# Kernel tuning notes

Hardware: AMD Instinct MI355X
Metric: run time of the kernel (lower is better)

Reference implementation:

```python
import jax, jax.numpy as jnp
import numpy as np

N_NODES = 50000
N_EDGES = 800000
IN_CH = 128
HID = 32
HEADS = 4
OUT_CH = 64
N_GRAPHS = 64


def setup_inputs() -> dict:
    key = jax.random.key(0)
    ks = jax.random.split(key, 16)
    x = jax.random.normal(ks[0], (N_NODES, IN_CH), dtype=jnp.float32)
    edge_index = jax.random.randint(ks[1], (2, N_EDGES), 0, N_NODES, dtype=jnp.int64)
    edge_attr = jax.random.normal(ks[2], (N_EDGES, 8), dtype=jnp.float32)
    nodeIDs = jnp.sort(jax.random.randint(ks[3], (N_NODES,), 0, N_GRAPHS, dtype=jnp.int64))
    s = 0.1
    W1 = jax.random.normal(ks[4], (IN_CH, HEADS * HID), dtype=jnp.float32) * s
    att_src1 = jax.random.normal(ks[5], (HEADS, HID), dtype=jnp.float32) * s
    att_dst1 = jax.random.normal(ks[6], (HEADS, HID), dtype=jnp.float32) * s
    b1 = jax.random.normal(ks[7], (HEADS * HID,), dtype=jnp.float32) * s
    W2 = jax.random.normal(ks[8], (HEADS * HID, 16), dtype=jnp.float32) * s
    att_src2 = jax.random.normal(ks[9], (1, 16), dtype=jnp.float32) * s
    att_dst2 = jax.random.normal(ks[10], (1, 16), dtype=jnp.float32) * s
    b2 = jax.random.normal(ks[11], (16,), dtype=jnp.float32) * s
    Wf = jax.random.normal(ks[12], (16, OUT_CH), dtype=jnp.float32) * s
    bf = jax.random.normal(ks[13], (OUT_CH,), dtype=jnp.float32) * s
    return dict(x=x, edge_index=edge_index, edge_attr=edge_attr, nodeIDs=nodeIDs,
                W1=W1, att_src1=att_src1, att_dst1=att_dst1, b1=b1,
                W2=W2, att_src2=att_src2, att_dst2=att_dst2, b2=b2,
                Wf=Wf, bf=bf)


def gat_conv(x, src, dst, n, W, a_src, a_dst, b, heads, out_ch, concat):
    # linear transform -> [N, H, C]
    h = (x @ W).reshape(n, heads, out_ch)
    # per-node attention logits [N, H]
    asrc = jnp.sum(h * a_src, axis=-1)
    adst = jnp.sum(h * a_dst, axis=-1)
    e = jax.nn.leaky_relu(asrc[src] + adst[dst], 0.2)  # [E, H]
    # segment softmax over edges sharing the same destination node
    m = jax.ops.segment_max(e, dst, num_segments=n)
    e = jnp.exp(e - m[dst])
    s = jax.ops.segment_sum(e, dst, num_segments=n)
    alpha = e / (s[dst] + 1e-16)
    # weighted scatter-add aggregation: [N, H, C]
    out = jax.ops.segment_sum(alpha[:, :, None] * h[src], dst, num_segments=n)
    out = out.reshape(n, heads * out_ch) if concat else out.mean(axis=1)
    return out + b


def reference(x, edge_index, edge_attr, nodeIDs, W1, att_src1, att_dst1, b1,
              W2, att_src2, att_dst2, b2, Wf, bf):
    n = x.shape[0]
    # GATConv default: add self-loops
    loop = jnp.arange(n, dtype=edge_index.dtype)
    src = jnp.concatenate([edge_index[0], loop])
    dst = jnp.concatenate([edge_index[1], loop])
    # eval mode: dropout is identity. edge_attr ignored (no edge_dim in GATConv).
    h = jax.nn.relu(gat_conv(x, src, dst, n, W1, att_src1, att_dst1, b1, HEADS, HID, True))
    h = jax.nn.relu(gat_conv(h, src, dst, n, W2, att_src2, att_dst2, b2, 1, 16, False))
    # global mean pool over graphs
    sums = jax.ops.segment_sum(h, nodeIDs, num_segments=N_GRAPHS)
    cnts = jax.ops.segment_sum(jnp.ones((n,), dtype=h.dtype), nodeIDs, num_segments=N_GRAPHS)
    pooled = sums / jnp.maximum(cnts, 1.0)[:, None]  # [G, 16]
    return pooled @ Wf + bf
```

## Files before the change

kernel.cpp:

```cpp
#include <hip/hip_runtime.h>
#include <hip/hip_bf16.h>
#include <hip/hip_fp16.h>


__device__ __forceinline__ float lrelu02(float x) { return x > 0.f ? x : 0.2f * x; }

union H16 { _Float16 h; unsigned short u; };
__device__ __forceinline__ unsigned short f2h(float f) { H16 t; t.h = (_Float16)f; return t.u; }
__device__ __forceinline__ float h2f(unsigned short u) { H16 t; t.u = u; return (float)t.h; }

typedef __attribute__((ext_vector_type(8))) _Float16 half8v;
typedef __attribute__((ext_vector_type(4))) float f32x4;

#define CAP 64
#define CSTRIDE 16

__global__ __launch_bounds__(256) void k_bucket(
    const float* __restrict__ W1, const float* __restrict__ W2,
    unsigned short* __restrict__ W1th, unsigned short* __restrict__ W2th,
    const int* __restrict__ src, const int* __restrict__ dst,
    int* __restrict__ cnt, unsigned short* __restrict__ bkt, int E, int N)
{
    if ((int)blockIdx.x < 144) {
        if (threadIdx.x < 128) {
            int b = blockIdx.x, k = threadIdx.x;
            if (b < 128) W1th[b * 128 + k] = f2h(W1[k * 128 + b]);
            else { int c = b - 128; W2th[c * 128 + k] = f2h(W2[k * 16 + c]); }
        }
        return;
    }
    const int b  = blockIdx.x - 144;
    const int g  = b & 7;
    const int lo = (int)(((long long)N * g) >> 3);
    const int hi = (int)(((long long)N * (g + 1)) >> 3);
    const int nb = 2048 >> 3;
    const int bi = b >> 3;
    const int E4 = E >> 2;
    const int4* dst4 = (const int4*)dst;
    const int4* src4 = (const int4*)src;
    for (int i = bi * 256 + threadIdx.x; i < E4; i += nb * 256) {
        int4 d4 = dst4[i];
        int4 s4 = src4[i];
        if (d4.x >= lo && d4.x < hi) {
            int slot = atomicAdd(&cnt[d4.x * CSTRIDE], 1);
            if (slot < CAP) bkt[(d4.x << 6) + slot] = (unsigned short)s4.x;
        }
        if (d4.y >= lo && d4.y < hi) {
            int slot = atomicAdd(&cnt[d4.y * CSTRIDE], 1);
            if (slot < CAP) bkt[(d4.y << 6) + slot] = (unsigned short)s4.y;
        }
        if (d4.z >= lo && d4.z < hi) {
            int slot = atomicAdd(&cnt[d4.z * CSTRIDE], 1);
            if (slot < CAP) bkt[(d4.z << 6) + slot] = (unsigned short)s4.z;
        }
        if (d4.w >= lo && d4.w < hi) {
            int slot = atomicAdd(&cnt[d4.w * CSTRIDE], 1);
            if (slot < CAP) bkt[(d4.w << 6) + slot] = (unsigned short)s4.w;
        }
    }
    for (int i = E4 * 4 + bi * 256 + threadIdx.x; i < E; i += nb * 256) {
        int d = dst[i];
        if (d >= lo && d < hi) {
            int slot = atomicAdd(&cnt[d * CSTRIDE], 1);
            if (slot < CAP) bkt[(d << 6) + slot] = (unsigned short)src[i];
        }
    }
}

__global__ __launch_bounds__(256) void k_gemm1(
    const float* __restrict__ x, const unsigned short* __restrict__ W1th,
    const float* __restrict__ a_src, const float* __restrict__ a_dst,
    unsigned short* __restrict__ H1h, float* __restrict__ asrcv, float* __restrict__ adstv, int N)
{
    __shared__ unsigned short sL[4][16][136];
    const int tid = threadIdx.x;
    const int w  = tid >> 6, l = tid & 63;
    const int mr = l & 15, kg = l >> 4;
    const int m0 = w * 16;
    const int rowbase = blockIdx.x * 64;

    const int grow_a = rowbase + m0 + mr;
    const float* xr = x + (size_t)(grow_a < N ? grow_a : N - 1) * 128;

    f32x4 acc[8];
#pragma unroll
    for (int nt = 0; nt < 8; ++nt) acc[nt] = (f32x4){0.f, 0.f, 0.f, 0.f};

#pragma unroll
    for (int kk = 0; kk < 4; ++kk) {
        const int kbase = kk * 32 + kg * 8;
        float4 xa = *(const float4*)(xr + kbase);
        float4 xb = *(const float4*)(xr + kbase + 4);
        half8v a;
        a[0] = (_Float16)xa.x; a[1] = (_Float16)xa.y;
        a[2] = (_Float16)xa.z; a[3] = (_Float16)xa.w;
        a[4] = (_Float16)xb.x; a[5] = (_Float16)xb.y;
        a[6] = (_Float16)xb.z; a[7] = (_Float16)xb.w;
#pragma unroll
        for (int nt = 0; nt < 8; ++nt) {
            half8v b = *(const half8v*)&W1th[(size_t)(nt * 16 + mr) * 128 + kbase];
            acc[nt] = __builtin_amdgcn_mfma_f32_16x16x32_f16(a, b, acc[nt], 0, 0, 0);
        }
    }

    {
        float as_[8], ad_[8];
#pragma unroll
        for (int nt = 0; nt < 8; ++nt) { as_[nt] = a_src[nt * 16 + mr]; ad_[nt] = a_dst[nt * 16 + mr]; }
#pragma unroll
        for (int j = 0; j < 4; ++j) {
            float vs[4], vd[4];
#pragma unroll
            for (int h = 0; h < 4; ++h) {
                vs[h] = acc[2 * h][j] * as_[2 * h] + acc[2 * h + 1][j] * as_[2 * h + 1];
                vd[h] = acc[2 * h][j] * ad_[2 * h] + acc[2 * h + 1][j] * ad_[2 * h + 1];
#pragma unroll
                for (int xm = 1; xm <= 8; xm <<= 1) {
                    vs[h] += __shfl_xor(vs[h], xm);
                    vd[h] += __shfl_xor(vd[h], xm);
                }
            }
            int grow = rowbase + m0 + kg * 4 + j;
            if (mr == 0 && grow < N) {
                *(float4*)&asrcv[grow * 4] = make_float4(vs[0], vs[1], vs[2], vs[3]);
                *(float4*)&adstv[grow * 4] = make_float4(vd[0], vd[1], vd[2], vd[3]);
            }
        }
    }

#pragma unroll
    for (int nt = 0; nt < 8; ++nt)
#pragma unroll
        for (int j = 0; j < 4; ++j)
            sL[w][kg * 4 + j][nt * 16 + mr] = f2h(acc[nt][j]);
    {
        int r = l >> 2, k0 = (l & 3) * 32;
        int grow = rowbase + m0 + r;
        if (grow < N) {
            const uint4* sp = (const uint4*)&sL[w][r][k0];
            uint4* dp = (uint4*)&H1h[(size_t)grow * 128 + k0];
#pragma unroll
            for (int q = 0; q < 4; ++q) dp[q] = sp[q];
        }
    }
}

__global__ __launch_bounds__(256) void k_agg1(
    const unsigned short* __restrict__ H1h, const float* __restrict__ asrc, const float* __restrict__ adst,
    const int* __restrict__ cnt, const unsigned short* __restrict__ bkt,
    const float* __restrict__ b1, unsigned short* __restrict__ out1h, int N)
{
    __shared__ float sEs[4][64 * 4];
    __shared__ int   sSs[4][64];
    const int w = threadIdx.x >> 6, lane = threadIdx.x & 63;
    float* sE = sEs[w];
    int*   sS = sSs[w];
    const int n = blockIdx.x * 4 + w;
    if (n >= N) return;
    const int deg = min(cnt[n * CSTRIDE], CAP);

    const float4 ad4 = *(const float4*)&adst[n * 4];
    const float4 as4 = *(const float4*)&asrc[n * 4];
    float es0 = __expf(lrelu02(as4.x + ad4.x));
    float es1 = __expf(lrelu02(as4.y + ad4.y));
    float es2 = __expf(lrelu02(as4.z + ad4.z));
    float es3 = __expf(lrelu02(as4.w + ad4.w));
    float ssum0 = es0, ssum1 = es1, ssum2 = es2, ssum3 = es3;
    if (lane != 0) { ssum0 = 0.f; ssum1 = 0.f; ssum2 = 0.f; ssum3 = 0.f; }

    const int g = lane >> 4, q = lane & 15;
    const int c0 = q * 8, h = q >> 2;
    float acc[8] = {0.f,0.f,0.f,0.f,0.f,0.f,0.f,0.f};

    if (lane < deg) {
        int s = (int)bkt[(n << 6) + lane];
        sS[lane] = s;
        const float4 a = *(const float4*)&asrc[s * 4];
        float e0 = __expf(lrelu02(a.x + ad4.x));
        float e1 = __expf(lrelu02(a.y + ad4.y));
        float e2 = __expf(lrelu02(a.z + ad4.z));
        float e3 = __expf(lrelu02(a.w + ad4.w));
        ssum0 += e0; ssum1 += e1; ssum2 += e2; ssum3 += e3;
        sE[lane * 4 + 0] = e0; sE[lane * 4 + 1] = e1;
        sE[lane * 4 + 2] = e2; sE[lane * 4 + 3] = e3;
    }
    union U8 { uint4 u; _Float16 hh[8]; };
    for (int j = g; j < deg; j += 4) {
        int s = sS[j];
        float e = sE[j * 4 + h];
        U8 uu; uu.u = *(const uint4*)&H1h[(size_t)s * 128 + c0];
#pragma unroll
        for (int k = 0; k < 8; ++k)
            acc[k] = fmaf(e, (float)uu.hh[k], acc[k]);
    }

#pragma unroll
    for (int xm = 32; xm >= 1; xm >>= 1) {
        ssum0 += __shfl_xor(ssum0, xm);
        ssum1 += __shfl_xor(ssum1, xm);
        ssum2 += __shfl_xor(ssum2, xm);
        ssum3 += __shfl_xor(ssum3, xm);
    }
#pragma unroll
    for (int k = 0; k < 8; ++k) {
        acc[k] += __shfl_xor(acc[k], 16);
        acc[k] += __shfl_xor(acc[k], 32);
    }
    if (g == 0) {
        float ssv = (h == 0) ? ssum0 : (h == 1) ? ssum1 : (h == 2) ? ssum2 : ssum3;
        float esv = (h == 0) ? es0   : (h == 1) ? es1   : (h == 2) ? es2   : es3;
        float inv = 1.f / (ssv + 1e-16f);
        U8 uu; uu.u = *(const uint4*)&H1h[(size_t)n * 128 + c0];
        const float4 ba = *(const float4*)&b1[c0];
        const float4 bb = *(const float4*)&b1[c0 + 4];
        float o[8];
#pragma unroll
        for (int k = 0; k < 8; ++k) o[k] = (acc[k] + esv * (float)uu.hh[k]) * inv;
        o[0] = fmaxf(o[0] + ba.x, 0.f); o[1] = fmaxf(o[1] + ba.y, 0.f);
        o[2] = fmaxf(o[2] + ba.z, 0.f); o[3] = fmaxf(o[3] + ba.w, 0.f);
        o[4] = fmaxf(o[4] + bb.x, 0.f); o[5] = fmaxf(o[5] + bb.y, 0.f);
        o[6] = fmaxf(o[6] + bb.z, 0.f); o[7] = fmaxf(o[7] + bb.w, 0.f);
        uint2 pk0, pk1;
        pk0.x = (unsigned)f2h(o[0]) | ((unsigned)f2h(o[1]) << 16);
        pk0.y = (unsigned)f2h(o[2]) | ((unsigned)f2h(o[3]) << 16);
        pk1.x = (unsigned)f2h(o[4]) | ((unsigned)f2h(o[5]) << 16);
        pk1.y = (unsigned)f2h(o[6]) | ((unsigned)f2h(o[7]) << 16);
        *(uint2*)&out1h[(size_t)n * 128 + c0]     = pk0;
        *(uint2*)&out1h[(size_t)n * 128 + c0 + 4] = pk1;
    }
}

__global__ __launch_bounds__(256) void k_gemm2m(
    const unsigned short* __restrict__ X1h, const unsigned short* __restrict__ W2th,
    const float* __restrict__ a_src2, const float* __restrict__ a_dst2,
    unsigned short* __restrict__ H2h, float* __restrict__ asrcv, float* __restrict__ adstv, int N)
{
    const int tid = threadIdx.x;
    const int w = tid >> 6, l = tid & 63;
    const int mr = l & 15, kg = l >> 4;
    const int rowbase = blockIdx.x * 64 + w * 16;
    const int grow_a = rowbase + mr;
    const unsigned short* xr = X1h + (size_t)(grow_a < N ? grow_a : N - 1) * 128;

    f32x4 acc = (f32x4){0.f, 0.f, 0.f, 0.f};
#pragma unroll
    for (int kk = 0; kk < 4; ++kk) {
        const int kbase = kk * 32 + kg * 8;
        half8v a = *(const half8v*)&xr[kbase];
        half8v b = *(const half8v*)&W2th[mr * 128 + kbase];
        acc = __builtin_amdgcn_mfma_f32_16x16x32_f16(a, b, acc, 0, 0, 0);
    }
    const float as_ = a_src2[mr], ad_ = a_dst2[mr];
#pragma unroll
    for (int j = 0; j < 4; ++j) {
        float vs = acc[j] * as_;
        float vd = acc[j] * ad_;
#pragma unroll
        for (int xm = 1; xm <= 8; xm <<= 1) { vs += __shfl_xor(vs, xm); vd += __shfl_xor(vd, xm); }
        int grow = rowbase + kg * 4 + j;
        if (grow < N) {
            H2h[(size_t)grow * 16 + mr] = f2h(acc[j]);
            if (mr == 0) { asrcv[grow] = vs; adstv[grow] = vd; }
        }
    }
}

__global__ __launch_bounds__(256) void k_agg2(
    const unsigned short* __restrict__ H2h, const float* __restrict__ asrc, const float* __restrict__ adst,
    const int* __restrict__ cnt, const unsigned short* __restrict__ bkt,
    float* __restrict__ out, int N)
{
    __shared__ float sEs[4][64];
    __shared__ int   sSs[4][64];
    const int w = threadIdx.x >> 6, lane = threadIdx.x & 63;
    float* sE = sEs[w];
    int*   sS = sSs[w];
    const int n = blockIdx.x * 4 + w;
    if (n >= N) return;
    const int deg = min(cnt[n * CSTRIDE], CAP);

    const float adv = adst[n];
    float eself = __expf(lrelu02(asrc[n] + adv));
    float ssum = (lane == 0) ? eself : 0.f;

    const int g = lane >> 3, q = lane & 7;
    const int c0 = q * 2;
    float acc0 = 0.f, acc1 = 0.f;

    if (lane < deg) {
        int s = (int)bkt[(n << 6) + lane];
        sS[lane] = s;
        float e = __expf(lrelu02(asrc[s] + adv));
        ssum += e;
        sE[lane] = e;
    }
    union U2 { unsigned u; _Float16 hh[2]; };
    for (int j = g; j < deg; j += 8) {
        int s = sS[j];
        float e = sE[j];
        U2 uu; uu.u = *(const unsigned*)&H2h[(size_t)s * 16 + c0];
        acc0 = fmaf(e, (float)uu.hh[0], acc0);
        acc1 = fmaf(e, (float)uu.hh[1], acc1);
    }
#pragma unroll
    for (int xm = 32; xm >= 1; xm >>= 1) ssum += __shfl_xor(ssum, xm);
    acc0 += __shfl_xor(acc0, 8);  acc1 += __shfl_xor(acc1, 8);
    acc0 += __shfl_xor(acc0, 16); acc1 += __shfl_xor(acc1, 16);
    acc0 += __shfl_xor(acc0, 32); acc1 += __shfl_xor(acc1, 32);
    if (g == 0) {
        float inv = 1.f / (ssum + 1e-16f);
        U2 uu; uu.u = *(const unsigned*)&H2h[(size_t)n * 16 + c0];
        float2 o;
        o.x = (acc0 + eself * (float)uu.hh[0]) * inv;
        o.y = (acc1 + eself * (float)uu.hh[1]) * inv;
        *(float2*)&out[(size_t)n * 16 + c0] = o;
    }
}

__global__ __launch_bounds__(256) void k_poolfinal(
    const float* __restrict__ out2, const float* __restrict__ b2,
    const int* __restrict__ nodeIDs, const float* __restrict__ Wf,
    const float* __restrict__ bf, float* __restrict__ outp, int N)
{
    int g = blockIdx.x;
    int lo = 0, hi = N;
    while (lo < hi) { int mid = (lo + hi) >> 1; if (nodeIDs[mid] < g) lo = mid + 1; else hi = mid; }
    int start = lo;
    lo = 0; hi = N;
    while (lo < hi) { int mid = (lo + hi) >> 1; if (nodeIDs[mid] < g + 1) lo = mid + 1; else hi = mid; }
    int end = lo;

    int c = threadIdx.x & 15, grp = threadIdx.x >> 4;
    float bc = b2[c];
    float acc = 0.f;
    for (int n = start + grp; n < end; n += 16)
        acc += fmaxf(out2[(size_t)n * 16 + c] + bc, 0.f);

    __shared__ float sd[256];
    __shared__ float p16[16];
    sd[threadIdx.x] = acc;
    __syncthreads();
#pragma unroll
    for (int s = 8; s >= 1; s >>= 1) {
        if (grp < s) sd[threadIdx.x] += sd[(grp + s) * 16 + c];
        __syncthreads();
    }
    if (threadIdx.x < 16) {
        float cnt_ = (float)(end - start);
        p16[threadIdx.x] = sd[threadIdx.x] / fmaxf(cnt_, 1.f);
    }
    __syncthreads();
    if (threadIdx.x < 64) {
        int o = threadIdx.x;
        float a = bf[o];
#pragma unroll
        for (int k = 0; k < 16; ++k)
            a = fmaf(p16[k], Wf[k * 64 + o], a);
        outp[(size_t)g * 64 + o] = a;
    }
}

extern "C" void kernel_launch(void* const* d_in, const int* in_sizes, int n_in,
                              void* d_out, int out_size, void* d_ws, size_t ws_size,
                              hipStream_t stream)
{
    const float* x   = (const float*)d_in[0];
    const int*   ei  = (const int*)  d_in[1];
    const int*   nid = (const int*)  d_in[3];
    const float* W1  = (const float*)d_in[4];
    const float* as1 = (const float*)d_in[5];
    const float* ad1 = (const float*)d_in[6];
    const float* b1  = (const float*)d_in[7];
    const float* W2  = (const float*)d_in[8];
    const float* as2 = (const float*)d_in[9];
    const float* ad2 = (const float*)d_in[10];
    const float* b2  = (const float*)d_in[11];
    const float* Wf  = (const float*)d_in[12];
    const float* bf  = (const float*)d_in[13];
    float* outp = (float*)d_out;

    const int N = in_sizes[0] / 128;
    const int E = in_sizes[1] / 2;
    const int* src = ei;
    const int* dst = ei + E;

    char* ws = (char*)d_ws;
    size_t off_b = 0;
    auto alloc = [&](size_t bytes) -> char* {
        char* p = ws + off_b;
        off_b += (bytes + 255) & ~(size_t)255;
        return p;
    };

    unsigned short* H1h   = (unsigned short*)alloc((size_t)N * 128 * 2);
    unsigned short* out1h = (unsigned short*)alloc((size_t)N * 128 * 2);
    unsigned short* H2h   = (unsigned short*)alloc((size_t)N * 16 * 2);
    unsigned short* bkt   = (unsigned short*)alloc((size_t)N * CAP * 2);
    unsigned short* W1th  = (unsigned short*)alloc((size_t)128 * 128 * 2);
    unsigned short* W2th  = (unsigned short*)alloc((size_t)16 * 128 * 2);
    float* asrc1  = (float*)alloc((size_t)N * 4 * 4);
    float* adst1  = (float*)alloc((size_t)N * 4 * 4);
    float* out2   = (float*)alloc((size_t)N * 16 * 4);
    float* asrc2  = (float*)alloc((size_t)N * 4);
    float* adst2  = (float*)alloc((size_t)N * 4);
    int*   cnt    = (int*)  alloc((size_t)N * CSTRIDE * 4);

    auto cdiv = [](long long a, long long b) { return (int)((a + b - 1) / b); };

    const int GB = cdiv(N, 64);

    hipMemsetAsync(cnt, 0, (size_t)N * CSTRIDE * 4, stream);

    k_bucket<<<144 + 2048, 256, 0, stream>>>(W1, W2, W1th, W2th,
                                             src, dst, cnt, bkt, E, N);

    k_gemm1<<<GB, 256, 0, stream>>>(x, W1th, as1, ad1, H1h, asrc1, adst1, N);

    k_agg1<<<cdiv(N, 4), 256, 0, stream>>>(H1h, asrc1, adst1, cnt, bkt, b1, out1h, N);

    k_gemm2m<<<cdiv(N, 64), 256, 0, stream>>>(out1h, W2th, as2, ad2, H2h, asrc2, adst2, N);

    k_agg2<<<cdiv(N, 4), 256, 0, stream>>>(H2h, asrc2, adst2, cnt, bkt, out2, N);

    k_poolfinal<<<out_size / 64, 256, 0, stream>>>(out2, b2, nid, Wf, bf, outp, N);
}
```

Measured before the change: 155.7 us.

## Fuse mean-pool into layer-2 aggregation with atomics and use persistent grid-stride agg kernels

Layer-2 aggregation now applies bias and ReLU and atomically accumulates per-graph sums and counts, so the out2 buffer and the pool kernel's re-read go away. A small final kernel does the 16x64 projection. Both aggregation kernels become persistent grid-stride loops over 2048 blocks. They also pack the precomputed byte offset and the attention weight into one LDS uint2. The risk is heavy atomic contention on only 64 graphs times 16 channels, which also makes the float sum order nondeterministic.

Result: slower. 447.0 us (+187.1%).

```diff
diff --git a/kernel.cpp b/kernel.cpp
--- a/kernel.cpp
+++ b/kernel.cpp
@@ -7,7 +7,6 @@
 
 union H16 { _Float16 h; unsigned short u; };
 __device__ __forceinline__ unsigned short f2h(float f) { H16 t; t.h = (_Float16)f; return t.u; }
-__device__ __forceinline__ float h2f(unsigned short u) { H16 t; t.u = u; return (float)t.h; }
 
 typedef __attribute__((ext_vector_type(8))) _Float16 half8v;
 typedef __attribute__((ext_vector_type(4))) float f32x4;
@@ -150,83 +149,88 @@
     const int* __restrict__ cnt, const unsigned short* __restrict__ bkt,
     const float* __restrict__ b1, unsigned short* __restrict__ out1h, int N)
 {
-    __shared__ float sEs[4][64 * 4];
-    __shared__ int   sSs[4][64];
+    __shared__ uint2 sPs[4][64][4];
     const int w = threadIdx.x >> 6, lane = threadIdx.x & 63;
-    float* sE = sEs[w];
-    int*   sS = sSs[w];
-    const int n = blockIdx.x * 4 + w;
-    if (n >= N) return;
-    const int deg = min(cnt[n * CSTRIDE], CAP);
-
-    const float4 ad4 = *(const float4*)&adst[n * 4];
-    const float4 as4 = *(const float4*)&asrc[n * 4];
-    float es0 = __expf(lrelu02(as4.x + ad4.x));
-    float es1 = __expf(lrelu02(as4.y + ad4.y));
-    float es2 = __expf(lrelu02(as4.z + ad4.z));
-    float es3 = __expf(lrelu02(as4.w + ad4.w));
-    float ssum0 = es0, ssum1 = es1, ssum2 = es2, ssum3 = es3;
-    if (lane != 0) { ssum0 = 0.f; ssum1 = 0.f; ssum2 = 0.f; ssum3 = 0.f; }
-
+    uint2 (*sP)[4] = sPs[w];
     const int g = lane >> 4, q = lane & 15;
     const int c0 = q * 8, h = q >> 2;
-    float acc[8] = {0.f,0.f,0.f,0.f,0.f,0.f,0.f,0.f};
-
-    if (lane < deg) {
-        int s = (int)bkt[(n << 6) + lane];
-        sS[lane] = s;
-        const float4 a = *(const float4*)&asrc[s * 4];
-        float e0 = __expf(lrelu02(a.x + ad4.x));
-        float e1 = __expf(lrelu02(a.y + ad4.y));
-        float e2 = __expf(lrelu02(a.z + ad4.z));
-        float e3 = __expf(lrelu02(a.w + ad4.w));
-        ssum0 += e0; ssum1 += e1; ssum2 += e2; ssum3 += e3;
-        sE[lane * 4 + 0] = e0; sE[lane * 4 + 1] = e1;
-        sE[lane * 4 + 2] = e2; sE[lane * 4 + 3] = e3;
-    }
+    const int laneoff = c0 * 2;
+    const float4 ba = *(const float4*)&b1[c0];
+    const float4 bb = *(const float4*)&b1[c0 + 4];
+    const int wid = blockIdx.x * 4 + w;
+    const int nw  = gridDim.x * 4;
+    const char* H1c = (const char*)H1h;
+
     union U8 { uint4 u; _Float16 hh[8]; };
-    for (int j = g; j < deg; j += 4) {
-        int s = sS[j];
-        float e = sE[j * 4 + h];
-        U8 uu; uu.u = *(const uint4*)&H1h[(size_t)s * 128 + c0];
-#pragma unroll
-        for (int k = 0; k < 8; ++k)
-            acc[k] = fmaf(e, (float)uu.hh[k], acc[k]);
-    }
-
-#pragma unroll
-    for (int xm = 32; xm >= 1; xm >>= 1) {
-        ssum0 += __shfl_xor(ssum0, xm);
-        ssum1 += __shfl_xor(ssum1, xm);
-        ssum2 += __shfl_xor(ssum2, xm);
-        ssum3 += __shfl_xor(ssum3, xm);
-    }
-#pragma unroll
-    for (int k = 0; k < 8; ++k) {
-        acc[k] += __shfl_xor(acc[k], 16);
-        acc[k] += __shfl_xor(acc[k], 32);
-    }
-    if (g == 0) {
-        float ssv = (h == 0) ? ssum0 : (h == 1) ? ssum1 : (h == 2) ? ssum2 : ssum3;
-        float esv = (h == 0) ? es0   : (h == 1) ? es1   : (h == 2) ? es2   : es3;
-        float inv = 1.f / (ssv + 1e-16f);
-        U8 uu; uu.u = *(const uint4*)&H1h[(size_t)n * 128 + c0];
-        const float4 ba = *(const float4*)&b1[c0];
-        const float4 bb = *(const float4*)&b1[c0 + 4];
-        float o[8];
-#pragma unroll
-        for (int k = 0; k < 8; ++k) o[k] = (acc[k] + esv * (float)uu.hh[k]) * inv;
-        o[0] = fmaxf(o[0] + ba.x, 0.f); o[1] = fmaxf(o[1] + ba.y, 0.f);
-        o[2] = fmaxf(o[2] + ba.z, 0.f); o[3] = fmaxf(o[3] + ba.w, 0.f);
-        o[4] = fmaxf(o[4] + bb.x, 0.f); o[5] = fmaxf(o[5] + bb.y, 0.f);
-        o[6] = fmaxf(o[6] + bb.z, 0.f); o[7] = fmaxf(o[7] + bb.w, 0.f);
-        uint2 pk0, pk1;
-        pk0.x = (unsigned)f2h(o[0]) | ((unsigned)f2h(o[1]) << 16);
-        pk0.y = (unsigned)f2h(o[2]) | ((unsigned)f2h(o[3]) << 16);
-        pk1.x = (unsigned)f2h(o[4]) | ((unsigned)f2h(o[5]) << 16);
-        pk1.y = (unsigned)f2h(o[6]) | ((unsigned)f2h(o[7]) << 16);
-        *(uint2*)&out1h[(size_t)n * 128 + c0]     = pk0;
-        *(uint2*)&out1h[(size_t)n * 128 + c0 + 4] = pk1;
+
+    for (int n = wid; n < N; n += nw) {
+        const int deg = min(cnt[n * CSTRIDE], CAP);
+        const float4 ad4 = *(const float4*)&adst[n * 4];
+        const float4 as4 = *(const float4*)&asrc[n * 4];
+        float es0 = __expf(lrelu02(as4.x + ad4.x));
+        float es1 = __expf(lrelu02(as4.y + ad4.y));
+        float es2 = __expf(lrelu02(as4.z + ad4.z));
+        float es3 = __expf(lrelu02(as4.w + ad4.w));
+        float ssum0 = es0, ssum1 = es1, ssum2 = es2, ssum3 = es3;
+        if (lane != 0) { ssum0 = 0.f; ssum1 = 0.f; ssum2 = 0.f; ssum3 = 0.f; }
+
+        float acc[8] = {0.f,0.f,0.f,0.f,0.f,0.f,0.f,0.f};
+
+        if (lane < deg) {
+            int s = (int)bkt[(n << 6) + lane];
+            unsigned ab = (unsigned)s << 8;
+            const float4 a = *(const float4*)&asrc[s * 4];
+            float e0 = __expf(lrelu02(a.x + ad4.x));
+            float e1 = __expf(lrelu02(a.y + ad4.y));
+            float e2 = __expf(lrelu02(a.z + ad4.z));
+            float e3 = __expf(lrelu02(a.w + ad4.w));
+            ssum0 += e0; ssum1 += e1; ssum2 += e2; ssum3 += e3;
+            sP[lane][0] = make_uint2(ab, __float_as_uint(e0));
+            sP[lane][1] = make_uint2(ab, __float_as_uint(e1));
+            sP[lane][2] = make_uint2(ab, __float_as_uint(e2));
+            sP[lane][3] = make_uint2(ab, __float_as_uint(e3));
+        }
+        for (int j = g; j < deg; j += 4) {
+            uint2 p = sP[j][h];
+            U8 uu; uu.u = *(const uint4*)(H1c + p.x + laneoff);
+            float e = __uint_as_float(p.y);
+#pragma unroll
+            for (int k = 0; k < 8; ++k)
+                acc[k] = fmaf(e, (float)uu.hh[k], acc[k]);
+        }
+
+#pragma unroll
+        for (int xm = 32; xm >= 1; xm >>= 1) {
+            ssum0 += __shfl_xor(ssum0, xm);
+            ssum1 += __shfl_xor(ssum1, xm);
+            ssum2 += __shfl_xor(ssum2, xm);
+            ssum3 += __shfl_xor(ssum3, xm);
+        }
+#pragma unroll
+        for (int k = 0; k < 8; ++k) {
+            acc[k] += __shfl_xor(acc[k], 16);
+            acc[k] += __shfl_xor(acc[k], 32);
+        }
+        if (g == 0) {
+            float ssv = (h == 0) ? ssum0 : (h == 1) ? ssum1 : (h == 2) ? ssum2 : ssum3;
+            float esv = (h == 0) ? es0   : (h == 1) ? es1   : (h == 2) ? es2   : es3;
+            float inv = 1.f / (ssv + 1e-16f);
+            U8 uu; uu.u = *(const uint4*)&H1h[(size_t)n * 128 + c0];
+            float o[8];
+#pragma unroll
+            for (int k = 0; k < 8; ++k) o[k] = (acc[k] + esv * (float)uu.hh[k]) * inv;
+            o[0] = fmaxf(o[0] + ba.x, 0.f); o[1] = fmaxf(o[1] + ba.y, 0.f);
+            o[2] = fmaxf(o[2] + ba.z, 0.f); o[3] = fmaxf(o[3] + ba.w, 0.f);
+            o[4] = fmaxf(o[4] + bb.x, 0.f); o[5] = fmaxf(o[5] + bb.y, 0.f);
+            o[6] = fmaxf(o[6] + bb.z, 0.f); o[7] = fmaxf(o[7] + bb.w, 0.f);
+            uint2 pk0, pk1;
+            pk0.x = (unsigned)f2h(o[0]) | ((unsigned)f2h(o[1]) << 16);
+            pk0.y = (unsigned)f2h(o[2]) | ((unsigned)f2h(o[3]) << 16);
+            pk1.x = (unsigned)f2h(o[4]) | ((unsigned)f2h(o[5]) << 16);
+            pk1.y = (unsigned)f2h(o[6]) | ((unsigned)f2h(o[7]) << 16);
+            *(uint2*)&out1h[(size_t)n * 128 + c0]     = pk0;
+            *(uint2*)&out1h[(size_t)n * 128 + c0 + 4] = pk1;
+        }
     }
 }
 
@@ -268,96 +272,74 @@
 __global__ __launch_bounds__(256) void k_agg2(
     const unsigned short* __restrict__ H2h, const float* __restrict__ asrc, const float* __restrict__ adst,
     const int* __restrict__ cnt, const unsigned short* __restrict__ bkt,
-    float* __restrict__ out, int N)
-{
-    __shared__ float sEs[4][64];
-    __shared__ int   sSs[4][64];
+    const int* __restrict__ nid, const float* __restrict__ b2,
+    float* __restrict__ pooled, int* __restrict__ pcnt, int N)
+{
+    __shared__ uint2 sPs[4][64];
     const int w = threadIdx.x >> 6, lane = threadIdx.x & 63;
-    float* sE = sEs[w];
-    int*   sS = sSs[w];
-    const int n = blockIdx.x * 4 + w;
-    if (n >= N) return;
-    const int deg = min(cnt[n * CSTRIDE], CAP);
-
-    const float adv = adst[n];
-    float eself = __expf(lrelu02(asrc[n] + adv));
-    float ssum = (lane == 0) ? eself : 0.f;
-
+    uint2* sP = sPs[w];
     const int g = lane >> 3, q = lane & 7;
     const int c0 = q * 2;
-    float acc0 = 0.f, acc1 = 0.f;
-
-    if (lane < deg) {
-        int s = (int)bkt[(n << 6) + lane];
-        sS[lane] = s;
-        float e = __expf(lrelu02(asrc[s] + adv));
-        ssum += e;
-        sE[lane] = e;
-    }
+    const int laneoff = c0 * 2;
+    const float b2x = b2[c0], b2y = b2[c0 + 1];
+    const int wid = blockIdx.x * 4 + w;
+    const int nw  = gridDim.x * 4;
+    const char* H2c = (const char*)H2h;
+
     union U2 { unsigned u; _Float16 hh[2]; };
-    for (int j = g; j < deg; j += 8) {
-        int s = sS[j];
-        float e = sE[j];
-        U2 uu; uu.u = *(const unsigned*)&H2h[(size_t)s * 16 + c0];
-        acc0 = fmaf(e, (float)uu.hh[0], acc0);
-        acc1 = fmaf(e, (float)uu.hh[1], acc1);
-    }
-#pragma unroll
-    for (int xm = 32; xm >= 1; xm >>= 1) ssum += __shfl_xor(ssum, xm);
-    acc0 += __shfl_xor(acc0, 8);  acc1 += __shfl_xor(acc1, 8);
-    acc0 += __shfl_xor(acc0, 16); acc1 += __shfl_xor(acc1, 16);
-    acc0 += __shfl_xor(acc0, 32); acc1 += __shfl_xor(acc1, 32);
-    if (g == 0) {
-        float inv = 1.f / (ssum + 1e-16f);
-        U2 uu; uu.u = *(const unsigned*)&H2h[(size_t)n * 16 + c0];
-        float2 o;
-        o.x = (acc0 + eself * (float)uu.hh[0]) * inv;
-        o.y = (acc1 + eself * (float)uu.hh[1]) * inv;
-        *(float2*)&out[(size_t)n * 16 + c0] = o;
-    }
-}
-
-__global__ __launch_bounds__(256) void k_poolfinal(
-    const float* __restrict__ out2, const float* __restrict__ b2,
-    const int* __restrict__ nodeIDs, const float* __restrict__ Wf,
-    const float* __restrict__ bf, float* __restrict__ outp, int N)
-{
-    int g = blockIdx.x;
-    int lo = 0, hi = N;
-    while (lo < hi) { int mid = (lo + hi) >> 1; if (nodeIDs[mid] < g) lo = mid + 1; else hi = mid; }
-    int start = lo;
-    lo = 0; hi = N;
-    while (lo < hi) { int mid = (lo + hi) >> 1; if (nodeIDs[mid] < g + 1) lo = mid + 1; else hi = mid; }
-    int end = lo;
-
-    int c = threadIdx.x & 15, grp = threadIdx.x >> 4;
-    float bc = b2[c];
-    float acc = 0.f;
-    for (int n = start + grp; n < end; n += 16)
-        acc += fmaxf(out2[(size_t)n * 16 + c] + bc, 0.f);
-
-    __shared__ float sd[256];
-    __shared__ float p16[16];
-    sd[threadIdx.x] = acc;
-    __syncthreads();
-#pragma unroll
-    for (int s = 8; s >= 1; s >>= 1) {
-        if (grp < s) sd[threadIdx.x] += sd[(grp + s) * 16 + c];
-        __syncthreads();
-    }
-    if (threadIdx.x < 16) {
-        float cnt_ = (float)(end - start);
-        p16[threadIdx.x] = sd[threadIdx.x] / fmaxf(cnt_, 1.f);
-    }
-    __syncthreads();
-    if (threadIdx.x < 64) {
-        int o = threadIdx.x;
-        float a = bf[o];
-#pragma unroll
-        for (int k = 0; k < 16; ++k)
-            a = fmaf(p16[k], Wf[k * 64 + o], a);
-        outp[(size_t)g * 64 + o] = a;
-    }
+
+    for (int n = wid; n < N; n += nw) {
+        const int deg = min(cnt[n * CSTRIDE], CAP);
+        const float adv = adst[n];
+        float eself = __expf(lrelu02(asrc[n] + adv));
+        float ssum = (lane == 0) ? eself : 0.f;
+        float acc0 = 0.f, acc1 = 0.f;
+
+        if (lane < deg) {
+            int s = (int)bkt[(n << 6) + lane];
+            float e = __expf(lrelu02(asrc[s] + adv));
+            ssum += e;
+            sP[lane] = make_uint2((unsigned)s << 5, __float_as_uint(e));
+        }
+        for (int j = g; j < deg; j += 8) {
+            uint2 p = sP[j];
+            U2 uu; uu.u = *(const unsigned*)(H2c + p.x + laneoff);
+            float e = __uint_as_float(p.y);
+            acc0 = fmaf(e, (float)uu.hh[0], acc0);
+            acc1 = fmaf(e, (float)uu.hh[1], acc1);
+        }
+#pragma unroll
+        for (int xm = 32; xm >= 1; xm >>= 1) ssum += __shfl_xor(ssum, xm);
+        acc0 += __shfl_xor(acc0, 8);  acc1 += __shfl_xor(acc1, 8);
+        acc0 += __shfl_xor(acc0, 16); acc1 += __shfl_xor(acc1, 16);
+        acc0 += __shfl_xor(acc0, 32); acc1 += __shfl_xor(acc1, 32);
+        if (g == 0) {
+            float inv = 1.f / (ssum + 1e-16f);
+            U2 uu; uu.u = *(const unsigned*)&H2h[(size_t)n * 16 + c0];
+            float ox = fmaxf((acc0 + eself * (float)uu.hh[0]) * inv + b2x, 0.f);
+            float oy = fmaxf((acc1 + eself * (float)uu.hh[1]) * inv + b2y, 0.f);
+            int gid = nid[n];
+            atomicAdd(&pooled[gid * 16 + c0],     ox);
+            atomicAdd(&pooled[gid * 16 + c0 + 1], oy);
+            if (q == 0) atomicAdd(&pcnt[gid], 1);
+        }
+    }
+}
+
+__global__ __launch_bounds__(256) void k_final(
+    const float* __restrict__ pooled, const int* __restrict__ pcnt,
+    const float* __restrict__ Wf, const float* __restrict__ bf,
+    float* __restrict__ outp, int G)
+{
+    int i = blockIdx.x * 256 + threadIdx.x;
+    if (i >= G * 64) return;
+    int g = i >> 6, o = i & 63;
+    float invc = 1.f / fmaxf((float)pcnt[g], 1.f);
+    float acc = bf[o];
+#pragma unroll
+    for (int k = 0; k < 16; ++k)
+        acc = fmaf(pooled[g * 16 + k] * invc, Wf[k * 64 + o], acc);
+    outp[i] = acc;
 }
 
 extern "C" void kernel_launch(void* const* d_in, const int* in_sizes, int n_in,
@@ -381,6 +363,7 @@
 
     const int N = in_sizes[0] / 128;
     const int E = in_sizes[1] / 2;
+    const int G = out_size / 64;
     const int* src = ei;
     const int* dst = ei + E;
 
@@ -400,27 +383,30 @@
     unsigned short* W2th  = (unsigned short*)alloc((size_t)16 * 128 * 2);
     float* asrc1  = (float*)alloc((size_t)N * 4 * 4);
     float* adst1  = (float*)alloc((size_t)N * 4 * 4);
-    float* out2   = (float*)alloc((size_t)N * 16 * 4);
     float* asrc2  = (float*)alloc((size_t)N * 4);
     float* adst2  = (float*)alloc((size_t)N * 4);
+    size_t zstart = off_b;
     int*   cnt    = (int*)  alloc((size_t)N * CSTRIDE * 4);
+    float* pooled = (float*)alloc((size_t)G * 16 * 4);
+    int*   pcnt   = (int*)  alloc((size_t)G * 4);
+    size_t zbytes = off_b - zstart;
 
     auto cdiv = [](long long a, long long b) { return (int)((a + b - 1) / b); };
 
     const int GB = cdiv(N, 64);
 
-    hipMemsetAsync(cnt, 0, (size_t)N * CSTRIDE * 4, stream);
+    hipMemsetAsync(ws + zstart, 0, zbytes, stream);
 
     k_bucket<<<144 + 2048, 256, 0, stream>>>(W1, W2, W1th, W2th,
                                              src, dst, cnt, bkt, E, N);
 
     k_gemm1<<<GB, 256, 0, stream>>>(x, W1th, as1, ad1, H1h, asrc1, adst1, N);
 
-    k_agg1<<<cdiv(N, 4), 256, 0, stream>>>(H1h, asrc1, adst1, cnt, bkt, b1, out1h, N);
+    k_agg1<<<2048, 256, 0, stream>>>(H1h, asrc1, adst1, cnt, bkt, b1, out1h, N);
 
     k_gemm2m<<<cdiv(N, 64), 256, 0, stream>>>(out1h, W2th, as2, ad2, H2h, asrc2, adst2, N);
 
-    k_agg2<<<cdiv(N, 4), 256, 0, stream>>>(H2h, asrc2, adst2, cnt, bkt, out2, N);
-
-    k_poolfinal<<<out_size / 64, 256, 0, stream>>>(out2, b2, nid, Wf, bf, outp, N);
-}
+    k_agg2<<<2048, 256, 0, stream>>>(H2h, asrc2, adst2, cnt, bkt, nid, b2, pooled, pcnt, N);
+
+    k_final<<<cdiv((long long)G * 64, 256), 256, 0, stream>>>(pooled, pcnt, Wf, bf, outp, G);
+}
```
